# Performance work log

Hardware: AMD Instinct MI355X
Metric: run time of the kernel (lower is better)

## Reference

```python
import jax, jax.numpy as jnp
import numpy as np

MAX_DISP = 4  # displacement radius -> 9x9 = 81 shifts


def setup_inputs() -> dict:
    key = jax.random.key(0)
    k1, k2 = jax.random.split(key)
    B, C, H, W = 8, 256, 96, 160
    tensorFirst = jax.random.normal(k1, (B, C, H, W), dtype=jnp.float32)
    tensorSecond = jax.random.normal(k2, (B, C, H, W), dtype=jnp.float32)
    return {"tensorFirst": tensorFirst, "tensorSecond": tensorSecond}


def reference(tensorFirst, tensorSecond):
    # Multi-displacement cross-correlation cost volume (FlowNet/PWC-Net style).
    # For each of the 81 displacements (dy, dx) in [-4, 4]^2:
    #   out[b, i*9+j, y, x] = mean_c( input1[b,c,y,x] * input2[b,c,y+dy,x+dx] )
    # (zero-padded outside the image), matching the torch fallback exactly
    # (sum over channels / channels == mean over channels).
    B, C, H, W = tensorFirst.shape
    p2 = jnp.pad(
        tensorSecond,
        ((0, 0), (0, 0), (MAX_DISP, MAX_DISP), (MAX_DISP, MAX_DISP)),
    )
    outs = []
    for dy in range(-MAX_DISP, MAX_DISP + 1):  # fixed 9-step loop (static shifts)
        for dx in range(-MAX_DISP, MAX_DISP + 1):
            shifted = p2[:, :, MAX_DISP + dy:MAX_DISP + dy + H,
                         MAX_DISP + dx:MAX_DISP + dx + W]
            outs.append(jnp.mean(tensorFirst * shifted, axis=1))  # [B, H, W]
    return jnp.stack(outs, axis=1)  # [B, 81, H, W]
```

## Files before the change

kernel.cpp:

```cpp
#include <hip/hip_runtime.h>
#include <hip/hip_fp16.h>

#define CH 256
#define HH 96
#define WW 160
#define HW (HH * WW)

typedef _Float16 h4 __attribute__((ext_vector_type(4)));
typedef float f32x4 __attribute__((ext_vector_type(4)));

__device__ inline unsigned pk2f(float a, float b) {
    return (unsigned)__half_as_ushort(__float2half(a)) |
           ((unsigned)__half_as_ushort(__float2half(b)) << 16);
}

__global__ __launch_bounds__(256, 4)
void corr_v5(const float* __restrict__ Fp, const float* __restrict__ Sp,
             float* __restrict__ out) {
    __shared__ uint2 sS[2 * 12 * 128];

    const int bid = blockIdx.x;
    const int b   = bid & 7;
    const int rem = bid >> 3;
    const int y0  = (rem / 10) * 4;
    const int x0  = (rem % 10) * 16;

    const int t    = threadIdx.x;
    const int lane = t & 63;
    const int wv   = t >> 6;
    const int q    = lane >> 4;
    const int n    = lane & 15;

    const float*  Fb  = Fp + (size_t)b * CH * HW;
    const float2* Sb2 = (const float2*)(Sp + (size_t)b * CH * HW);

    const int np = lane & 7;
    const int qq = (lane >> 3) & 3;
    const int jt = (lane >> 5) & 1;
    const int gx = x0 - 4 + jt * 16 + np * 2;
    const bool xok = (gx >= 0) & (gx + 1 < WW);

    bool okv[3];
    int  sOff[3];
#pragma unroll
    for (int i = 0; i < 3; i++) {
        const int row = i * 4 + wv;
        const int gy  = y0 - 4 + row;
        okv[i] = ((unsigned)gy < HH) & xok;
        sOff[i] = okv[i] ? (qq * 4) * (HW / 2) + gy * (WW / 2) + (gx >> 1) : 0;
    }
    int fOff = (q * 4) * HW + (y0 + wv) * WW + x0 + n;

    float2 rawS[3][4];
    float  rawF[4];
    h4     av;

    auto load_raw = [&]() {
#pragma unroll
        for (int i = 0; i < 3; i++)
#pragma unroll
            for (int j = 0; j < 4; j++)
                rawS[i][j] = Sb2[sOff[i] + j * (HW / 2)];
#pragma unroll
        for (int j = 0; j < 4; j++)
            rawF[j] = Fb[fOff + j * HW];
#pragma unroll
        for (int i = 0; i < 3; i++) sOff[i] += 8 * HW;
        fOff += 16 * HW;
    };

    const int wrow = jt * 64 + qq * 16 + np * 2;

    auto commit = [&](int wb) {
        h4 a;
#pragma unroll
        for (int j = 0; j < 4; j++) a[j] = (_Float16)rawF[j];
        av = a;
#pragma unroll
        for (int i = 0; i < 3; i++) {
            float ax[4], ay[4];
#pragma unroll
            for (int j = 0; j < 4; j++) {
                ax[j] = okv[i] ? rawS[i][j].x : 0.0f;
                ay[j] = okv[i] ? rawS[i][j].y : 0.0f;
            }
            uint4 v;
            v.x = pk2f(ax[0], ax[1]);
            v.y = pk2f(ax[2], ax[3]);
            v.z = pk2f(ay[0], ay[1]);
            v.w = pk2f(ay[2], ay[3]);
            *(uint4*)&sS[wb + (i * 4 + wv) * 128 + wrow] = v;
        }
    };

    f32x4 acc[9][2];
#pragma unroll
    for (int dy = 0; dy < 9; dy++) {
        f32x4 z = {0.f, 0.f, 0.f, 0.f};
        acc[dy][0] = z;
        acc[dy][1] = z;
    }

    load_raw();
    commit(0);
    load_raw();
    __syncthreads();

#pragma unroll 1
    for (int ch = 0; ch < 16; ch++) {
        const int rb = (ch & 1) ? 1536 : 0;
        const uint2* rp = sS + rb + wv * 128 + q * 16 + n;

#pragma unroll
        for (int dy = 0; dy < 9; dy++) {
            h4 b0 = *(const h4*)(rp + dy * 128);
            h4 b1 = *(const h4*)(rp + dy * 128 + 64);
            acc[dy][0] = __builtin_amdgcn_mfma_f32_16x16x16f16(av, b0, acc[dy][0], 0, 0, 0);
            acc[dy][1] = __builtin_amdgcn_mfma_f32_16x16x16f16(av, b1, acc[dy][1], 0, 0, 0);
        }

        if (ch < 15) {
            commit(1536 - rb);
            if (ch < 14) load_raw();
            __syncthreads();
        }
    }

    const int y = y0 + wv;
#pragma unroll
    for (int r = 0; r < 4; r++) {
        const int m = q * 4 + r;
#pragma unroll
        for (int jtt = 0; jtt < 2; jtt++) {
            const int dxp = jtt * 16 + n - m;
            if (dxp >= 0 && dxp <= 8) {
                float* p = out + ((size_t)(b * 81 + dxp) * HH + y) * WW + x0 + m;
#pragma unroll
                for (int dy = 0; dy < 9; dy++) {
                    p[(size_t)dy * 9 * HW] = acc[dy][jtt][r] * (1.0f / 256.0f);
                }
            }
        }
    }
}

extern "C" void kernel_launch(void* const* d_in, const int* in_sizes, int n_in,
                              void* d_out, int out_size, void* d_ws, size_t ws_size,
                              hipStream_t stream) {
    const float* F = (const float*)d_in[0];
    const float* S = (const float*)d_in[1];
    float* o = (float*)d_out;
    corr_v5<<<dim3(1920), dim3(256), 0, stream>>>(F, S, o);
}
```

Before: 328.6 us.

## Deepen register prefetch to two channel chunks with unrolled ping-pong loop

Keeps two sets of raw global-load registers (A and B), so loads for a chunk are issued two iterations ahead of when they are converted and written to shared memory. The main loop is unrolled by two so each LDS buffer and register set has a static role. The extra in-flight loads are meant to hide global memory latency further. The cost is more VGPRs, and the launch bound drops from 4 to 3 blocks per SM, which lowers occupancy.

```diff
diff --git a/kernel.cpp b/kernel.cpp
--- a/kernel.cpp
+++ b/kernel.cpp
@@ -14,8 +14,8 @@
            ((unsigned)__half_as_ushort(__float2half(b)) << 16);
 }
 
-__global__ __launch_bounds__(256, 4)
-void corr_v5(const float* __restrict__ Fp, const float* __restrict__ Sp,
+__global__ __launch_bounds__(256, 3)
+void corr_v6(const float* __restrict__ Fp, const float* __restrict__ Sp,
              float* __restrict__ out) {
     __shared__ uint2 sS[2 * 12 * 128];
 
@@ -51,19 +51,21 @@
     }
     int fOff = (q * 4) * HW + (y0 + wv) * WW + x0 + n;
 
-    float2 rawS[3][4];
-    float  rawF[4];
+    float2 rawSA[3][4];
+    float  rawFA[4];
+    float2 rawSB[3][4];
+    float  rawFB[4];
     h4     av;
 
-    auto load_raw = [&]() {
+    auto load_set = [&](float2 (&rS)[3][4], float (&rF)[4]) {
 #pragma unroll
         for (int i = 0; i < 3; i++)
 #pragma unroll
             for (int j = 0; j < 4; j++)
-                rawS[i][j] = Sb2[sOff[i] + j * (HW / 2)];
+                rS[i][j] = Sb2[sOff[i] + j * (HW / 2)];
 #pragma unroll
         for (int j = 0; j < 4; j++)
-            rawF[j] = Fb[fOff + j * HW];
+            rF[j] = Fb[fOff + j * HW];
 #pragma unroll
         for (int i = 0; i < 3; i++) sOff[i] += 8 * HW;
         fOff += 16 * HW;
@@ -71,18 +73,18 @@
 
     const int wrow = jt * 64 + qq * 16 + np * 2;
 
-    auto commit = [&](int wb) {
+    auto commit_set = [&](float2 (&rS)[3][4], float (&rF)[4], int wb) {
         h4 a;
 #pragma unroll
-        for (int j = 0; j < 4; j++) a[j] = (_Float16)rawF[j];
+        for (int j = 0; j < 4; j++) a[j] = (_Float16)rF[j];
         av = a;
 #pragma unroll
         for (int i = 0; i < 3; i++) {
             float ax[4], ay[4];
 #pragma unroll
             for (int j = 0; j < 4; j++) {
-                ax[j] = okv[i] ? rawS[i][j].x : 0.0f;
-                ay[j] = okv[i] ? rawS[i][j].y : 0.0f;
+                ax[j] = okv[i] ? rS[i][j].x : 0.0f;
+                ay[j] = okv[i] ? rS[i][j].y : 0.0f;
             }
             uint4 v;
             v.x = pk2f(ax[0], ax[1]);
@@ -101,28 +103,41 @@
         acc[dy][1] = z;
     }
 
-    load_raw();
-    commit(0);
-    load_raw();
+    load_set(rawSA, rawFA);
+    load_set(rawSB, rawFB);
+    commit_set(rawSA, rawFA, 0);
+    load_set(rawSA, rawFA);
     __syncthreads();
 
 #pragma unroll 1
-    for (int ch = 0; ch < 16; ch++) {
-        const int rb = (ch & 1) ? 1536 : 0;
-        const uint2* rp = sS + rb + wv * 128 + q * 16 + n;
-
+    for (int ch = 0; ch < 16; ch += 2) {
+        {
+            const uint2* rp = sS + wv * 128 + q * 16 + n;
 #pragma unroll
-        for (int dy = 0; dy < 9; dy++) {
-            h4 b0 = *(const h4*)(rp + dy * 128);
-            h4 b1 = *(const h4*)(rp + dy * 128 + 64);
-            acc[dy][0] = __builtin_amdgcn_mfma_f32_16x16x16f16(av, b0, acc[dy][0], 0, 0, 0);
-            acc[dy][1] = __builtin_amdgcn_mfma_f32_16x16x16f16(av, b1, acc[dy][1], 0, 0, 0);
+            for (int dy = 0; dy < 9; dy++) {
+                h4 b0 = *(const h4*)(rp + dy * 128);
+                h4 b1 = *(const h4*)(rp + dy * 128 + 64);
+                acc[dy][0] = __builtin_amdgcn_mfma_f32_16x16x16f16(av, b0, acc[dy][0], 0, 0, 0);
+                acc[dy][1] = __builtin_amdgcn_mfma_f32_16x16x16f16(av, b1, acc[dy][1], 0, 0, 0);
+            }
+            commit_set(rawSB, rawFB, 1536);
+            if (ch < 13) load_set(rawSB, rawFB);
+            __syncthreads();
         }
-
-        if (ch < 15) {
-            commit(1536 - rb);
-            if (ch < 14) load_raw();
-            __syncthreads();
+        {
+            const uint2* rp = sS + 1536 + wv * 128 + q * 16 + n;
+#pragma unroll
+            for (int dy = 0; dy < 9; dy++) {
+                h4 b0 = *(const h4*)(rp + dy * 128);
+                h4 b1 = *(const h4*)(rp + dy * 128 + 64);
+                acc[dy][0] = __builtin_amdgcn_mfma_f32_16x16x16f16(av, b0, acc[dy][0], 0, 0, 0);
+                acc[dy][1] = __builtin_amdgcn_mfma_f32_16x16x16f16(av, b1, acc[dy][1], 0, 0, 0);
+            }
+            if (ch < 14) {
+                commit_set(rawSA, rawFA, 0);
+                if (ch < 12) load_set(rawSA, rawFA);
+                __syncthreads();
+            }
         }
     }
 
@@ -150,5 +165,5 @@
     const float* F = (const float*)d_in[0];
     const float* S = (const float*)d_in[1];
     float* o = (float*)d_out;
-    corr_v5<<<dim3(1920), dim3(256), 0, stream>>>(F, S, o);
+    corr_v6<<<dim3(1920), dim3(256), 0, stream>>>(F, S, o);
 }
```

Measured after the change: 334.4 us. About the same (+1.8%).
